# Kernel tuning notes

Hardware: AMD Instinct MI355X
Metric: run time of the kernel (lower is better)

The kernel has to match this reference:

```python
import jax, jax.numpy as jnp
import numpy as np

D_MODEL = 1024
NUM_HEADS = 16
D_K = D_MODEL // NUM_HEADS


def setup_inputs() -> dict:
    key = jax.random.key(0)
    ks = jax.random.split(key, 8)
    B, S = 2, 2048
    query = jax.random.normal(ks[0], (B, S, D_MODEL), dtype=jnp.float32)
    k_in = jax.random.normal(ks[1], (B, S, D_MODEL), dtype=jnp.float32)
    value = jax.random.normal(ks[2], (B, S, D_MODEL), dtype=jnp.float32)
    # causal mask: True = masked out (upper triangle above diagonal)
    mask = jnp.triu(jnp.ones((S, S), dtype=bool), k=1)[None, None, :, :]
    scale = 1.0 / np.sqrt(D_MODEL)
    W_q = jax.random.normal(ks[3], (D_MODEL, D_MODEL), dtype=jnp.float32) * scale
    W_k = jax.random.normal(ks[4], (D_MODEL, D_MODEL), dtype=jnp.float32) * scale
    W_v = jax.random.normal(ks[5], (D_MODEL, D_MODEL), dtype=jnp.float32) * scale
    W_o = jax.random.normal(ks[6], (D_MODEL, D_MODEL), dtype=jnp.float32) * scale
    return {"query": query, "key": k_in, "value": value, "mask": mask,
            "W_q": W_q, "W_k": W_k, "W_v": W_v, "W_o": W_o}


def _split(x):
    # [B, S, d_model] -> [B, h, S, d_k]
    B, S, _ = x.shape
    return x.reshape(B, S, NUM_HEADS, D_K).transpose(0, 2, 1, 3)


def reference(query, key, value, mask, W_q, W_k, W_v, W_o):
    # torch nn.Linear(bias=False): y = x @ W.T
    Q = _split(query @ W_q.T)   # [B, h, Sq, d_k]
    K = _split(key @ W_k.T)     # [B, h, Sk, d_k]
    V = _split(value @ W_v.T)   # [B, h, Sk, d_k]
    scores = jnp.einsum('bhqd,bhkd->bhqk', Q, K) / jnp.sqrt(jnp.float32(D_K))
    scores = jnp.where(mask, -jnp.inf, scores)
    attn_w = jax.nn.softmax(scores, axis=-1)
    attn_w = jnp.nan_to_num(attn_w, nan=0.0)
    out = jnp.einsum('bhqk,bhkd->bhqd', attn_w, V)  # [B, h, Sq, d_k]
    B, _, Sq, _ = out.shape
    merged = out.transpose(0, 2, 1, 3).reshape(B, Sq, D_MODEL)
    return merged @ W_o.T
```

## Files before the change

kernel.cpp:

```cpp
#include <hip/hip_runtime.h>
#include <hip/hip_bf16.h>
#include <stdint.h>

typedef __attribute__((ext_vector_type(4))) float f32x4;
typedef __attribute__((ext_vector_type(8))) __bf16 bf16x8;
typedef __attribute__((ext_vector_type(4))) unsigned short us4;

#define SEQ 2048
#define DMODEL 1024
#define NH 16
#define DK 64
#define MTOT 4096

__device__ __forceinline__ unsigned short f2bf(float x) {
  union { float f; unsigned int u; } v; v.f = x;
  unsigned int r = v.u + 0x7fffu + ((v.u >> 16) & 1u);
  return (unsigned short)(r >> 16);
}

__device__ __forceinline__ unsigned int cvtpk(float lo, float hi) {
  unsigned int r;
  asm("v_cvt_pk_bf16_f32 %0, %1, %2" : "=v"(r) : "v"(lo), "v"(hi));
  return r;
}

__device__ __forceinline__ f32x4 mfma_bf16(bf16x8 a, bf16x8 b, f32x4 c) {
  return __builtin_amdgcn_mfma_f32_16x16x32_bf16(a, b, c, 0, 0, 0);
}

__device__ __forceinline__ void gload16(const void* g, void* l) {
  __builtin_amdgcn_global_load_lds((const __attribute__((address_space(1))) void*)g,
                                   (__attribute__((address_space(3))) void*)l,
                                   16, 0, 0);
}

__global__ void cvt_w(const float* __restrict__ s0, const float* __restrict__ s1,
                      const float* __restrict__ s2, const float* __restrict__ s3,
                      unsigned short* __restrict__ d0, unsigned short* __restrict__ d1,
                      unsigned short* __restrict__ d2, unsigned short* __restrict__ d3) {
  const int y = blockIdx.y;
  const float* s = y == 0 ? s0 : y == 1 ? s1 : y == 2 ? s2 : s3;
  unsigned short* d = y == 0 ? d0 : y == 1 ? d1 : y == 2 ? d2 : d3;
  const int n4 = DMODEL * DMODEL / 4;
  const int stride = gridDim.x * blockDim.x;
  for (int i = blockIdx.x * blockDim.x + threadIdx.x; i < n4; i += stride) {
    f32x4 v = reinterpret_cast<const f32x4*>(s)[i];
    us4 o;
    o.x = f2bf(v.x); o.y = f2bf(v.y); o.z = f2bf(v.z); o.w = f2bf(v.w);
    reinterpret_cast<us4*>(d)[i] = o;
  }
}

__global__ __launch_bounds__(256) void gemm_qkv(
    const float* __restrict__ xq, const float* __restrict__ xk, const float* __restrict__ xv,
    const unsigned short* __restrict__ bwq, const unsigned short* __restrict__ bwk,
    const unsigned short* __restrict__ bwv,
    unsigned short* __restrict__ Qh, unsigned short* __restrict__ Kh,
    unsigned short* __restrict__ Vt) {
  const int z = blockIdx.z;
  const float* A = z == 0 ? xq : (z == 1 ? xk : xv);
  const unsigned short* B = z == 0 ? bwq : (z == 1 ? bwk : bwv);
  const float scale = z == 0 ? 0.18033688011112042f : 1.0f;

  __shared__ __align__(16) float lAf[128 * 32];
  __shared__ __align__(16) unsigned short lB[64 * 64];
  const int tid = threadIdx.x;
  const int lane = tid & 63;
  const int wid = tid >> 6;
  const int l15 = lane & 15, l4 = lane >> 4;
  const int bm = blockIdx.x, bn = blockIdx.y;
  const int wr = wid >> 1, wc = wid & 1;

  f32x4 acc[4][4] = {};

  const float* gAsrc[4];
  float* lAdst[4];
#pragma unroll
  for (int is = 0; is < 4; ++is) {
    const int G = is * 256 + tid;
    const int row = G >> 3, pp = G & 7;
    const int lg = pp ^ (row & 7);
    gAsrc[is] = A + (size_t)(bm * 128 + row) * 1024 + lg * 4;
    lAdst[is] = lAf + (is * 256 + wid * 64) * 4;
  }
  const unsigned short* gBsrc[2];
  unsigned short* lBdst[2];
#pragma unroll
  for (int is = 0; is < 2; ++is) {
    const int G = is * 256 + tid;
    const int sr = G >> 3, pp = G & 7;
    const int lg = pp ^ (sr & 7);
    const int row = sr * 2 + (lg >> 2), kc = lg & 3;
    gBsrc[is] = B + (size_t)(bn * 128 + row) * 1024 + kc * 8;
    lBdst[is] = lB + (is * 256 + wid * 64) * 8;
  }

  for (int kt = 0; kt < 1024; kt += 32) {
    __syncthreads();
#pragma unroll
    for (int is = 0; is < 4; ++is) gload16(gAsrc[is] + kt, lAdst[is]);
#pragma unroll
    for (int is = 0; is < 2; ++is) gload16(gBsrc[is] + kt, lBdst[is]);
    __syncthreads();

    bf16x8 af[4], bfr[4];
#pragma unroll
    for (int i = 0; i < 4; ++i) {
      const int row = wr * 64 + i * 16 + l15;
      const int rb = row * 32, rx = row & 7;
      const f32x4 v0 = *reinterpret_cast<const f32x4*>(&lAf[rb + (((2 * l4 + 0) ^ rx) * 4)]);
      const f32x4 v1 = *reinterpret_cast<const f32x4*>(&lAf[rb + (((2 * l4 + 1) ^ rx) * 4)]);
      union { bf16x8 v; unsigned int u[4]; } t;
      t.u[0] = cvtpk(v0.x, v0.y);
      t.u[1] = cvtpk(v0.z, v0.w);
      t.u[2] = cvtpk(v1.x, v1.y);
      t.u[3] = cvtpk(v1.z, v1.w);
      af[i] = t.v;
    }
#pragma unroll
    for (int j = 0; j < 4; ++j) {
      const int row = wc * 64 + j * 16 + l15;
      const int sr = row >> 1;
      const int pp = (((row & 1) << 2) | l4) ^ (sr & 7);
      bfr[j] = *reinterpret_cast<const bf16x8*>(&lB[sr * 64 + pp * 8]);
    }
    if (z < 2) {
#pragma unroll
      for (int i = 0; i < 4; ++i)
#pragma unroll
        for (int j = 0; j < 4; ++j)
          acc[i][j] = mfma_bf16(bfr[j], af[i], acc[i][j]);
    } else {
#pragma unroll
      for (int i = 0; i < 4; ++i)
#pragma unroll
        for (int j = 0; j < 4; ++j)
          acc[i][j] = mfma_bf16(af[i], bfr[j], acc[i][j]);
    }
  }

  const int row0 = bm * 128 + wr * 64;
  const int col0 = bn * 128 + wc * 64;

  if (z < 2) {
    unsigned short* out = z ? Kh : Qh;
#pragma unroll
    for (int i = 0; i < 4; ++i) {
      const int m = row0 + i * 16 + l15;
      const int b = m >> 11, s = m & 2047;
#pragma unroll
      for (int j = 0; j < 4; ++j) {
        const int n0 = col0 + j * 16 + l4 * 4;
        const int h = n0 >> 6, dd = n0 & 63;
        union { us4 h4; unsigned int u[2]; } pk;
        pk.u[0] = cvtpk(acc[i][j][0] * scale, acc[i][j][1] * scale);
        pk.u[1] = cvtpk(acc[i][j][2] * scale, acc[i][j][3] * scale);
        *reinterpret_cast<us4*>(&out[(size_t)(b * NH + h) * (SEQ * DK) + s * DK + dd]) = pk.h4;
      }
    }
  } else {
#pragma unroll
    for (int i = 0; i < 4; ++i) {
      const int m0 = row0 + i * 16 + l4 * 4;
      const int b = m0 >> 11, s0 = m0 & 2047;
      const int g = (s0 >> 2) & 7;
      const int col = (s0 & ~31) + ((g & 3) << 3) + ((g >> 2) << 2);
#pragma unroll
      for (int j = 0; j < 4; ++j) {
        const int n = col0 + j * 16 + l15;
        const int h = n >> 6, dd = n & 63;
        union { us4 h4; unsigned int u[2]; } pk;
        pk.u[0] = cvtpk(acc[i][j][0], acc[i][j][1]);
        pk.u[1] = cvtpk(acc[i][j][2], acc[i][j][3]);
        *reinterpret_cast<us4*>(&Vt[(size_t)(b * NH + h) * (DK * SEQ) + dd * SEQ + col]) = pk.h4;
      }
    }
  }
}

__global__ __launch_bounds__(512) void gemm_o(const unsigned short* __restrict__ A,
                                              const unsigned short* __restrict__ B,
                                              float* __restrict__ out) {
  __shared__ __align__(16) unsigned short lA3[3][128 * 64];
  __shared__ __align__(16) unsigned short lB3[3][128 * 64];

  const int tid = threadIdx.x;
  const int lane = tid & 63, wid = tid >> 6;
  const int l15 = lane & 15, l4 = lane >> 4;
  const int bm = blockIdx.x, bn = blockIdx.y;
  const int wr = wid >> 1, wc = wid & 1;

  f32x4 acc[2][4] = {};

  const int r8 = lane >> 3, c8 = lane & 7;
  const unsigned short* gAs[2];
  const unsigned short* gBs[2];
  int dstoff[2];
#pragma unroll
  for (int is = 0; is < 2; ++is) {
    const int rbase = is * 64 + wid * 8;
    gAs[is] = A + (size_t)(bm * 128 + rbase + r8) * 1024 + (c8 ^ r8) * 8;
    gBs[is] = B + (size_t)(bn * 128 + rbase + r8) * 1024 + (c8 ^ r8) * 8;
    dstoff[is] = rbase * 64;
  }

#define STAGE_O(t, buf)                                         \
  {                                                             \
    const int kb = (t) * 64;                                    \
    gload16(gAs[0] + kb, &lA3[buf][dstoff[0]]);                 \
    gload16(gAs[1] + kb, &lA3[buf][dstoff[1]]);                 \
    gload16(gBs[0] + kb, &lB3[buf][dstoff[0]]);                 \
    gload16(gBs[1] + kb, &lB3[buf][dstoff[1]]);                 \
  }

  STAGE_O(0, 0);
  STAGE_O(1, 1);

#pragma unroll 1
  for (int t = 0; t < 16; ++t) {
    if (t + 1 < 16) {
      asm volatile("s_waitcnt vmcnt(4)" ::: "memory");
    } else {
      asm volatile("s_waitcnt vmcnt(0)" ::: "memory");
    }
    __builtin_amdgcn_sched_barrier(0);
    __builtin_amdgcn_s_barrier();
    __builtin_amdgcn_sched_barrier(0);

    if (t + 2 < 16) {
      const int pb = (t + 2) % 3;
      STAGE_O(t + 2, pb);
    }

    const unsigned short* La = lA3[t % 3];
    const unsigned short* Lb = lB3[t % 3];
#pragma unroll
    for (int kk = 0; kk < 2; ++kk) {
      bf16x8 af[2], bf[4];
#pragma unroll
      for (int i = 0; i < 2; ++i) {
        const int row = wr * 32 + i * 16 + l15;
        af[i] = *reinterpret_cast<const bf16x8*>(
            &La[row * 64 + (((kk * 4 + l4) ^ (l15 & 7)) * 8)]);
      }
#pragma unroll
      for (int j = 0; j < 4; ++j) {
        const int row = wc * 64 + j * 16 + l15;
        bf[j] = *reinterpret_cast<const bf16x8*>(
            &Lb[row * 64 + (((kk * 4 + l4) ^ (l15 & 7)) * 8)]);
      }
#pragma unroll
      for (int i = 0; i < 2; ++i)
#pragma unroll
        for (int j = 0; j < 4; ++j)
          acc[i][j] = mfma_bf16(bf[j], af[i], acc[i][j]);
    }
  }
#undef STAGE_O

  const int row0 = bm * 128 + wr * 32;
  const int col0 = bn * 128 + wc * 64;
#pragma unroll
  for (int i = 0; i < 2; ++i) {
    const int m = row0 + i * 16 + l15;
#pragma unroll
    for (int j = 0; j < 4; ++j) {
      const int n0 = col0 + j * 16 + l4 * 4;
      *reinterpret_cast<f32x4*>(&out[(size_t)m * DMODEL + n0]) = acc[i][j];
    }
  }
}

__global__ __launch_bounds__(512, 2) void attn_kernel(const unsigned short* __restrict__ Qh,
                                                      const unsigned short* __restrict__ Kh,
                                                      const unsigned short* __restrict__ Vt,
                                                      unsigned short* __restrict__ Mg) {
  __shared__ __align__(16) unsigned short Kl[4][64 * 64];
  __shared__ __align__(16) unsigned short Vl[4][64 * 64];

  const int tid = threadIdx.x;
  const int lane = tid & 63;
  const int w = tid >> 6;
  const int l15 = lane & 15, l4 = lane >> 4;

  const int d = blockIdx.x;
  const int base = d & 255;
  const int pair = d >> 8;
  const int xcd = base & 7;
  const int jj = base >> 3;
  const int bh = (jj >> 3) * 8 + xcd;
  const int qi = jj & 7;
  const int tau = pair ? qi : 15 - qi;

  const unsigned short* Qb = Qh + (size_t)bh * SEQ * DK;
  const unsigned short* Kb = Kh + (size_t)bh * SEQ * DK;
  const unsigned short* Vb = Vt + (size_t)bh * DK * SEQ;
  const int bq = bh >> 4, hh = bh & 15;
  unsigned short* Mbase = Mg + (size_t)bq * SEQ * DMODEL + hh * DK;

  const int srow = lane >> 3;
  const int sswz = (lane & 7) ^ srow;
  const unsigned short* KsrcB = Kb + (size_t)(w * 8 + srow) * DK + sswz * 8;
  const unsigned short* VsrcB = Vb + (size_t)(w * 8 + srow) * SEQ + sswz * 8;

  const int l7 = l15 & 7;

  const int qbase = tau * 128;
  const int q0w = qbase + w * 16;
  const int nt = 2 * tau + 2;

  bf16x8 qf0 = *reinterpret_cast<const bf16x8*>(Qb + (size_t)(q0w + l15) * DK + l4 * 8);
  bf16x8 qf1 = *reinterpret_cast<const bf16x8*>(Qb + (size_t)(q0w + l15) * DK + 32 + l4 * 8);

  f32x4 o[4] = {};
  float mrow = -__builtin_inff();
  float lrow = 0.0f;

  gload16(KsrcB, &Kl[0][w * 512]);
  gload16(VsrcB, &Vl[0][w * 512]);
  gload16(KsrcB + (size_t)64 * DK, &Kl[1][w * 512]);
  gload16(VsrcB + 64, &Vl[1][w * 512]);

  const int S = nt >> 1;
#pragma unroll 1
  for (int s = 0; s < S; ++s) {
    const int t0 = s << 1;
    const int kbase0 = t0 << 6;

    asm volatile("s_waitcnt vmcnt(0)" ::: "memory");
    __builtin_amdgcn_sched_barrier(0);
    __builtin_amdgcn_s_barrier();
    __builtin_amdgcn_sched_barrier(0);

    if (t0 + 2 < nt) {
      gload16(KsrcB + (size_t)(kbase0 + 128) * DK, &Kl[(t0 + 2) & 3][w * 512]);
      gload16(VsrcB + (kbase0 + 128), &Vl[(t0 + 2) & 3][w * 512]);
      gload16(KsrcB + (size_t)(kbase0 + 192) * DK, &Kl[(t0 + 3) & 3][w * 512]);
      gload16(VsrcB + (kbase0 + 192), &Vl[(t0 + 3) & 3][w * 512]);
    }

#pragma unroll
    for (int u = 0; u < 2; ++u) {
      const int t = t0 + u;
      const int kbase = t << 6;
      if (kbase >= q0w + 16) continue;
      const unsigned short* Kc = Kl[t & 3];
      const unsigned short* Vc = Vl[t & 3];

      f32x4 sc[4];
      __builtin_amdgcn_s_setprio(1);
#pragma unroll
      for (int c = 0; c < 4; ++c) {
        const int krow = c * 16 + l15;
        bf16x8 kf0 = *reinterpret_cast<const bf16x8*>(&Kc[krow * 64 + ((l4 ^ l7) * 8)]);
        bf16x8 kf1 = *reinterpret_cast<const bf16x8*>(&Kc[krow * 64 + (((4 + l4) ^ l7) * 8)]);
        f32x4 z = {0.f, 0.f, 0.f, 0.f};
        z = mfma_bf16(kf0, qf0, z);
        sc[c] = mfma_bf16(kf1, qf1, z);
      }
      __builtin_amdgcn_s_setprio(0);

      if (kbase + 63 > q0w) {
        const int qg = q0w + l15;
#pragma unroll
        for (int c = 0; c < 4; ++c) {
          const int kp = kbase + c * 16 + l4 * 4;
#pragma unroll
          for (int r = 0; r < 4; ++r)
            if (kp + r > qg) sc[c][r] = -__builtin_inff();
        }
      }

      f32x4 mv = sc[0];
#pragma unroll
      for (int c = 1; c < 4; ++c)
#pragma unroll
        for (int r = 0; r < 4; ++r) mv[r] = fmaxf(mv[r], sc[c][r]);
      float pm = fmaxf(fmaxf(mv[0], mv[1]), fmaxf(mv[2], mv[3]));
      if (!__all(pm - mrow <= 8.0f)) {
        pm = fmaxf(pm, __shfl_xor(pm, 16));
        pm = fmaxf(pm, __shfl_xor(pm, 32));
        const float mn = fmaxf(mrow, pm);
        const float al = __builtin_amdgcn_exp2f(mrow - mn);
        mrow = mn;
        lrow *= al;
#pragma unroll
        for (int dd = 0; dd < 4; ++dd)
#pragma unroll
          for (int r = 0; r < 4; ++r) o[dd][r] *= al;
      }
      union PB { bf16x8 v; unsigned int u[4]; } pbv[2];
      f32x4 sv = {0.f, 0.f, 0.f, 0.f};
#pragma unroll
      for (int c = 0; c < 4; ++c) {
        const float p0 = __builtin_amdgcn_exp2f(sc[c][0] - mrow);
        const float p1 = __builtin_amdgcn_exp2f(sc[c][1] - mrow);
        const float p2 = __builtin_amdgcn_exp2f(sc[c][2] - mrow);
        const float p3 = __builtin_amdgcn_exp2f(sc[c][3] - mrow);
        sv[0] += p0; sv[1] += p1; sv[2] += p2; sv[3] += p3;
        pbv[c >> 1].u[(c & 1) * 2 + 0] = cvtpk(p0, p1);
        pbv[c >> 1].u[(c & 1) * 2 + 1] = cvtpk(p2, p3);
      }
      lrow += (sv[0] + sv[1]) + (sv[2] + sv[3]);

      __builtin_amdgcn_s_setprio(1);
#pragma unroll
      for (int dd = 0; dd < 4; ++dd) {
        const int vrow = dd * 16 + l15;
#pragma unroll
        for (int p = 0; p < 2; ++p) {
          const bf16x8 av = *reinterpret_cast<const bf16x8*>(
              &Vc[vrow * 64 + (((p * 4 + l4) ^ l7) * 8)]);
          o[dd] = mfma_bf16(av, pbv[p].v, o[dd]);
        }
      }
      __builtin_amdgcn_s_setprio(0);
    }
  }

  lrow += __shfl_xor(lrow, 16);
  lrow += __shfl_xor(lrow, 32);
  const float inv = __builtin_amdgcn_rcpf(lrow);
  const int s = q0w + l15;
#pragma unroll
  for (int dd = 0; dd < 4; ++dd) {
    union { us4 h; unsigned int u[2]; } pk;
    pk.u[0] = cvtpk(o[dd][0] * inv, o[dd][1] * inv);
    pk.u[1] = cvtpk(o[dd][2] * inv, o[dd][3] * inv);
    *reinterpret_cast<us4*>(&Mbase[(size_t)s * DMODEL + dd * 16 + l4 * 4]) = pk.h;
  }
}

extern "C" void kernel_launch(void* const* d_in, const int* in_sizes, int n_in,
                              void* d_out, int out_size, void* d_ws, size_t ws_size,
                              hipStream_t stream) {
  (void)in_sizes; (void)n_in; (void)out_size;
  if (ws_size < (size_t)64 * (1 << 20)) return;

  const float* q = (const float*)d_in[0];
  const float* k = (const float*)d_in[1];
  const float* v = (const float*)d_in[2];
  const float* wq = (const float*)d_in[4];
  const float* wk = (const float*)d_in[5];
  const float* wv = (const float*)d_in[6];
  const float* wo = (const float*)d_in[7];

  char* ws = (char*)d_ws;
  unsigned short* bwq = (unsigned short*)(ws + (size_t)24 * (1 << 20));
  unsigned short* bwk = (unsigned short*)(ws + (size_t)26 * (1 << 20));
  unsigned short* bwv = (unsigned short*)(ws + (size_t)28 * (1 << 20));
  unsigned short* bwo = (unsigned short*)(ws + (size_t)30 * (1 << 20));
  unsigned short* Qh  = (unsigned short*)(ws + (size_t)32 * (1 << 20));
  unsigned short* Kh  = (unsigned short*)(ws + (size_t)40 * (1 << 20));
  unsigned short* Vt  = (unsigned short*)(ws + (size_t)48 * (1 << 20));
  unsigned short* Mg  = (unsigned short*)(ws + (size_t)56 * (1 << 20));

  cvt_w<<<dim3(64, 4), 256, 0, stream>>>(wq, wk, wv, wo, bwq, bwk, bwv, bwo);
  gemm_qkv<<<dim3(32, 8, 3), 256, 0, stream>>>(q, k, v, bwq, bwk, bwv, Qh, Kh, Vt);
  attn_kernel<<<dim3(512), 512, 0, stream>>>(Qh, Kh, Vt, Mg);
  gemm_o<<<dim3(32, 8), 512, 0, stream>>>(Mg, bwo, (float*)d_out);
}
```

Measured before the change: 133.5 us.

## Convert fp32 activations to bf16 on store to LDS, widen K tile, split V GEMM

```diff
diff --git a/kernel.cpp b/kernel.cpp
--- a/kernel.cpp
+++ b/kernel.cpp
@@ -5,6 +5,7 @@
 typedef __attribute__((ext_vector_type(4))) float f32x4;
 typedef __attribute__((ext_vector_type(8))) __bf16 bf16x8;
 typedef __attribute__((ext_vector_type(4))) unsigned short us4;
+typedef __attribute__((ext_vector_type(8))) unsigned short us8;
 
 #define SEQ 2048
 #define DMODEL 1024
@@ -28,8 +29,8 @@
   return __builtin_amdgcn_mfma_f32_16x16x32_bf16(a, b, c, 0, 0, 0);
 }
 
-__device__ __forceinline__ void gload16(const void* g, void* l) {
-  __builtin_amdgcn_global_load_lds((const __attribute__((address_space(1))) void*)g,
+__device__ __forceinline__ void gload16(const unsigned short* g, unsigned short* l) {
+  __builtin_amdgcn_global_load_lds((__attribute__((address_space(1))) void*)g,
                                    (__attribute__((address_space(3))) void*)l,
                                    16, 0, 0);
 }
@@ -51,19 +52,18 @@
   }
 }
 
-__global__ __launch_bounds__(256) void gemm_qkv(
-    const float* __restrict__ xq, const float* __restrict__ xk, const float* __restrict__ xv,
+__global__ __launch_bounds__(256) void gemm_qk(
+    const float* __restrict__ xq, const float* __restrict__ xk,
     const unsigned short* __restrict__ bwq, const unsigned short* __restrict__ bwk,
-    const unsigned short* __restrict__ bwv,
-    unsigned short* __restrict__ Qh, unsigned short* __restrict__ Kh,
-    unsigned short* __restrict__ Vt) {
+    unsigned short* __restrict__ Qh, unsigned short* __restrict__ Kh) {
   const int z = blockIdx.z;
-  const float* A = z == 0 ? xq : (z == 1 ? xk : xv);
-  const unsigned short* B = z == 0 ? bwq : (z == 1 ? bwk : bwv);
-  const float scale = z == 0 ? 0.18033688011112042f : 1.0f;
-
-  __shared__ __align__(16) float lAf[128 * 32];
-  __shared__ __align__(16) unsigned short lB[64 * 64];
+  const float* A = z ? xk : xq;
+  const unsigned short* B = z ? bwk : bwq;
+  unsigned short* out = z ? Kh : Qh;
+  const float scale = z ? 1.0f : 0.18033688011112042f;
+
+  __shared__ __align__(16) unsigned short lA[128 * 64];
+  __shared__ __align__(16) unsigned short lB[128 * 64];
   const int tid = threadIdx.x;
   const int lane = tid & 63;
   const int wid = tid >> 6;
@@ -73,64 +73,167 @@
 
   f32x4 acc[4][4] = {};
 
-  const float* gAsrc[4];
-  float* lAdst[4];
+  const int ar = tid >> 1, h = tid & 1;
+  const float* gAf = A + (size_t)(bm * 128 + ar) * 1024 + h * 32;
+  const int arx = ar & 7;
+  unsigned short* wA = lA + ar * 64;
+
+  const unsigned short* gBs[4];
+  unsigned short* lBd[4];
 #pragma unroll
   for (int is = 0; is < 4; ++is) {
     const int G = is * 256 + tid;
     const int row = G >> 3, pp = G & 7;
     const int lg = pp ^ (row & 7);
-    gAsrc[is] = A + (size_t)(bm * 128 + row) * 1024 + lg * 4;
-    lAdst[is] = lAf + (is * 256 + wid * 64) * 4;
-  }
-  const unsigned short* gBsrc[2];
-  unsigned short* lBdst[2];
-#pragma unroll
-  for (int is = 0; is < 2; ++is) {
-    const int G = is * 256 + tid;
-    const int sr = G >> 3, pp = G & 7;
-    const int lg = pp ^ (sr & 7);
-    const int row = sr * 2 + (lg >> 2), kc = lg & 3;
-    gBsrc[is] = B + (size_t)(bn * 128 + row) * 1024 + kc * 8;
-    lBdst[is] = lB + (is * 256 + wid * 64) * 8;
-  }
-
-  for (int kt = 0; kt < 1024; kt += 32) {
+    gBs[is] = B + (size_t)(bn * 128 + row) * 1024 + lg * 8;
+    lBd[is] = lB + (is * 256 + wid * 64) * 8;
+  }
+
+  f32x4 arg[8];
+#define QK_LOADA(kt_)                                                     \
+  {                                                                       \
+    _Pragma("unroll")                                                     \
+    for (int jj = 0; jj < 8; ++jj)                                        \
+      arg[jj] = *reinterpret_cast<const f32x4*>(gAf + (kt_) + jj * 4);    \
+  }
+
+  QK_LOADA(0);
+
+#pragma unroll 1
+  for (int kt = 0; kt < 1024; kt += 64) {
     __syncthreads();
 #pragma unroll
-    for (int is = 0; is < 4; ++is) gload16(gAsrc[is] + kt, lAdst[is]);
-#pragma unroll
-    for (int is = 0; is < 2; ++is) gload16(gBsrc[is] + kt, lBdst[is]);
+    for (int j = 0; j < 4; ++j) {
+      union { us8 v; unsigned int u[4]; } w;
+      w.u[0] = cvtpk(arg[2 * j][0], arg[2 * j][1]);
+      w.u[1] = cvtpk(arg[2 * j][2], arg[2 * j][3]);
+      w.u[2] = cvtpk(arg[2 * j + 1][0], arg[2 * j + 1][1]);
+      w.u[3] = cvtpk(arg[2 * j + 1][2], arg[2 * j + 1][3]);
+      const int pos = (h * 4 + j) ^ arx;
+      *reinterpret_cast<us8*>(wA + pos * 8) = w.v;
+    }
+#pragma unroll
+    for (int is = 0; is < 4; ++is) gload16(gBs[is] + kt, lBd[is]);
     __syncthreads();
 
-    bf16x8 af[4], bfr[4];
-#pragma unroll
-    for (int i = 0; i < 4; ++i) {
-      const int row = wr * 64 + i * 16 + l15;
-      const int rb = row * 32, rx = row & 7;
-      const f32x4 v0 = *reinterpret_cast<const f32x4*>(&lAf[rb + (((2 * l4 + 0) ^ rx) * 4)]);
-      const f32x4 v1 = *reinterpret_cast<const f32x4*>(&lAf[rb + (((2 * l4 + 1) ^ rx) * 4)]);
-      union { bf16x8 v; unsigned int u[4]; } t;
-      t.u[0] = cvtpk(v0.x, v0.y);
-      t.u[1] = cvtpk(v0.z, v0.w);
-      t.u[2] = cvtpk(v1.x, v1.y);
-      t.u[3] = cvtpk(v1.z, v1.w);
-      af[i] = t.v;
-    }
-#pragma unroll
-    for (int j = 0; j < 4; ++j) {
-      const int row = wc * 64 + j * 16 + l15;
-      const int sr = row >> 1;
-      const int pp = (((row & 1) << 2) | l4) ^ (sr & 7);
-      bfr[j] = *reinterpret_cast<const bf16x8*>(&lB[sr * 64 + pp * 8]);
-    }
-    if (z < 2) {
+    if (kt + 64 < 1024) QK_LOADA(kt + 64);
+
+#pragma unroll
+    for (int kk = 0; kk < 2; ++kk) {
+      bf16x8 af[4], bfr[4];
+#pragma unroll
+      for (int i = 0; i < 4; ++i) {
+        const int row = wr * 64 + i * 16 + l15;
+        af[i] = *reinterpret_cast<const bf16x8*>(
+            &lA[row * 64 + (((kk * 4 + l4) ^ (l15 & 7)) * 8)]);
+      }
+#pragma unroll
+      for (int j = 0; j < 4; ++j) {
+        const int row = wc * 64 + j * 16 + l15;
+        bfr[j] = *reinterpret_cast<const bf16x8*>(
+            &lB[row * 64 + (((kk * 4 + l4) ^ (l15 & 7)) * 8)]);
+      }
 #pragma unroll
       for (int i = 0; i < 4; ++i)
 #pragma unroll
         for (int j = 0; j < 4; ++j)
           acc[i][j] = mfma_bf16(bfr[j], af[i], acc[i][j]);
-    } else {
+    }
+  }
+#undef QK_LOADA
+
+  const int row0 = bm * 128 + wr * 64;
+  const int col0 = bn * 128 + wc * 64;
+#pragma unroll
+  for (int i = 0; i < 4; ++i) {
+    const int m = row0 + i * 16 + l15;
+    const int b = m >> 11, s = m & 2047;
+#pragma unroll
+    for (int j = 0; j < 4; ++j) {
+      const int n0 = col0 + j * 16 + l4 * 4;
+      const int hh = n0 >> 6, dd = n0 & 63;
+      union { us4 h4; unsigned int u[2]; } pk;
+      pk.u[0] = cvtpk(acc[i][j][0] * scale, acc[i][j][1] * scale);
+      pk.u[1] = cvtpk(acc[i][j][2] * scale, acc[i][j][3] * scale);
+      *reinterpret_cast<us4*>(&out[(size_t)(b * NH + hh) * (SEQ * DK) + s * DK + dd]) = pk.h4;
+    }
+  }
+}
+
+__global__ __launch_bounds__(256) void gemm_v(
+    const float* __restrict__ xv, const unsigned short* __restrict__ bwv,
+    unsigned short* __restrict__ Vt) {
+  __shared__ __align__(16) unsigned short lA[128 * 64];
+  __shared__ __align__(16) unsigned short lB[128 * 64];
+  const int tid = threadIdx.x;
+  const int lane = tid & 63;
+  const int wid = tid >> 6;
+  const int l15 = lane & 15, l4 = lane >> 4;
+  const int bm = blockIdx.x, bn = blockIdx.y;
+  const int wr = wid >> 1, wc = wid & 1;
+
+  f32x4 acc[4][4] = {};
+
+  const int ar = tid >> 1, h = tid & 1;
+  const float* gAf = xv + (size_t)(bm * 128 + ar) * 1024 + h * 32;
+  const int arx = ar & 7;
+  unsigned short* wA = lA + ar * 64;
+
+  const unsigned short* gBs[4];
+  unsigned short* lBd[4];
+#pragma unroll
+  for (int is = 0; is < 4; ++is) {
+    const int G = is * 256 + tid;
+    const int row = G >> 3, pp = G & 7;
+    const int lg = pp ^ (row & 7);
+    gBs[is] = bwv + (size_t)(bn * 128 + row) * 1024 + lg * 8;
+    lBd[is] = lB + (is * 256 + wid * 64) * 8;
+  }
+
+  f32x4 arg[8];
+#define V_LOADA(kt_)                                                      \
+  {                                                                       \
+    _Pragma("unroll")                                                     \
+    for (int jj = 0; jj < 8; ++jj)                                        \
+      arg[jj] = *reinterpret_cast<const f32x4*>(gAf + (kt_) + jj * 4);    \
+  }
+
+  V_LOADA(0);
+
+#pragma unroll 1
+  for (int kt = 0; kt < 1024; kt += 64) {
+    __syncthreads();
+#pragma unroll
+    for (int j = 0; j < 4; ++j) {
+      union { us8 v; unsigned int u[4]; } w;
+      w.u[0] = cvtpk(arg[2 * j][0], arg[2 * j][1]);
+      w.u[1] = cvtpk(arg[2 * j][2], arg[2 * j][3]);
+      w.u[2] = cvtpk(arg[2 * j + 1][0], arg[2 * j + 1][1]);
+      w.u[3] = cvtpk(arg[2 * j + 1][2], arg[2 * j + 1][3]);
+      const int pos = (h * 4 + j) ^ arx;
+      *reinterpret_cast<us8*>(wA + pos * 8) = w.v;
+    }
+#pragma unroll
+    for (int is = 0; is < 4; ++is) gload16(gBs[is] + kt, lBd[is]);
+    __syncthreads();
+
+    if (kt + 64 < 1024) V_LOADA(kt + 64);
+
+#pragma unroll
+    for (int kk = 0; kk < 2; ++kk) {
+      bf16x8 af[4], bfr[4];
+#pragma unroll
+      for (int i = 0; i < 4; ++i) {
+        const int row = wr * 64 + i * 16 + l15;
+        af[i] = *reinterpret_cast<const bf16x8*>(
+            &lA[row * 64 + (((kk * 4 + l4) ^ (l15 & 7)) * 8)]);
+      }
+#pragma unroll
+      for (int j = 0; j < 4; ++j) {
+        const int row = wc * 64 + j * 16 + l15;
+        bfr[j] = *reinterpret_cast<const bf16x8*>(
+            &lB[row * 64 + (((kk * 4 + l4) ^ (l15 & 7)) * 8)]);
+      }
 #pragma unroll
       for (int i = 0; i < 4; ++i)
 #pragma unroll
@@ -138,42 +241,24 @@
           acc[i][j] = mfma_bf16(af[i], bfr[j], acc[i][j]);
     }
   }
+#undef V_LOADA
 
   const int row0 = bm * 128 + wr * 64;
   const int col0 = bn * 128 + wc * 64;
-
-  if (z < 2) {
-    unsigned short* out = z ? Kh : Qh;
-#pragma unroll
-    for (int i = 0; i < 4; ++i) {
-      const int m = row0 + i * 16 + l15;
-      const int b = m >> 11, s = m & 2047;
-#pragma unroll
-      for (int j = 0; j < 4; ++j) {
-        const int n0 = col0 + j * 16 + l4 * 4;
-        const int h = n0 >> 6, dd = n0 & 63;
-        union { us4 h4; unsigned int u[2]; } pk;
-        pk.u[0] = cvtpk(acc[i][j][0] * scale, acc[i][j][1] * scale);
-        pk.u[1] = cvtpk(acc[i][j][2] * scale, acc[i][j][3] * scale);
-        *reinterpret_cast<us4*>(&out[(size_t)(b * NH + h) * (SEQ * DK) + s * DK + dd]) = pk.h4;
-      }
-    }
-  } else {
-#pragma unroll
-    for (int i = 0; i < 4; ++i) {
-      const int m0 = row0 + i * 16 + l4 * 4;
-      const int b = m0 >> 11, s0 = m0 & 2047;
-      const int g = (s0 >> 2) & 7;
-      const int col = (s0 & ~31) + ((g & 3) << 3) + ((g >> 2) << 2);
-#pragma unroll
-      for (int j = 0; j < 4; ++j) {
-        const int n = col0 + j * 16 + l15;
-        const int h = n >> 6, dd = n & 63;
-        union { us4 h4; unsigned int u[2]; } pk;
-        pk.u[0] = cvtpk(acc[i][j][0], acc[i][j][1]);
-        pk.u[1] = cvtpk(acc[i][j][2], acc[i][j][3]);
-        *reinterpret_cast<us4*>(&Vt[(size_t)(b * NH + h) * (DK * SEQ) + dd * SEQ + col]) = pk.h4;
-      }
+#pragma unroll
+  for (int i = 0; i < 4; ++i) {
+    const int m0 = row0 + i * 16 + l4 * 4;
+    const int b = m0 >> 11, s0 = m0 & 2047;
+    const int g = (s0 >> 2) & 7;
+    const int col = (s0 & ~31) + ((g & 3) << 3) + ((g >> 2) << 2);
+#pragma unroll
+    for (int j = 0; j < 4; ++j) {
+      const int n = col0 + j * 16 + l15;
+      const int hh = n >> 6, dd = n & 63;
+      union { us4 h4; unsigned int u[2]; } pk;
+      pk.u[0] = cvtpk(acc[i][j][0], acc[i][j][1]);
+      pk.u[1] = cvtpk(acc[i][j][2], acc[i][j][3]);
+      *reinterpret_cast<us4*>(&Vt[(size_t)(b * NH + hh) * (DK * SEQ) + dd * SEQ + col]) = pk.h4;
     }
   }
 }
@@ -456,7 +541,8 @@
   unsigned short* Mg  = (unsigned short*)(ws + (size_t)56 * (1 << 20));
 
   cvt_w<<<dim3(64, 4), 256, 0, stream>>>(wq, wk, wv, wo, bwq, bwk, bwv, bwo);
-  gemm_qkv<<<dim3(32, 8, 3), 256, 0, stream>>>(q, k, v, bwq, bwk, bwv, Qh, Kh, Vt);
+  gemm_qk<<<dim3(32, 8, 2), 256, 0, stream>>>(q, k, bwq, bwk, Qh, Kh);
+  gemm_v<<<dim3(32, 8), 256, 0, stream>>>(v, bwv, Vt);
   attn_kernel<<<dim3(512), 512, 0, stream>>>(Qh, Kh, Vt, Mg);
   gemm_o<<<dim3(32, 8), 512, 0, stream>>>(Mg, bwo, (float*)d_out);
 }
```

Result: slower. 140.5 us (+5.2%).
